# Kernel optimization log

Measured on AMD Instinct MI355X. Metric: run time of the kernel, lower is better.

The kernel has to match this reference:

```python
import jax, jax.numpy as jnp
import numpy as np

EMBED_DIM = 1024
NUM_HEADS = 16
HEAD_DIM = EMBED_DIM // NUM_HEADS
B, T = 4, 1024
NEG = -1.0e9
LN_EPS = 1e-5


def setup_inputs() -> dict:
    key = jax.random.key(0)
    ks = jax.random.split(key, 13)
    s = 1.0 / np.sqrt(EMBED_DIM)
    return {
        "query": jax.random.normal(ks[0], (B, T, EMBED_DIM), jnp.float32),
        "key": jax.random.normal(ks[1], (B, T, EMBED_DIM), jnp.float32),
        "value": jax.random.normal(ks[2], (B, T, EMBED_DIM), jnp.float32),
        "mask": jax.random.randint(ks[3], (B, 1, T, T), 0, 2, jnp.int32),
        "Wq": jax.random.normal(ks[4], (EMBED_DIM, EMBED_DIM), jnp.float32) * s,
        "bq": jnp.zeros((EMBED_DIM,), jnp.float32),
        "Wk": jax.random.normal(ks[5], (EMBED_DIM, EMBED_DIM), jnp.float32) * s,
        "bk": jnp.zeros((EMBED_DIM,), jnp.float32),
        "Wv": jax.random.normal(ks[6], (EMBED_DIM, EMBED_DIM), jnp.float32) * s,
        "bv": jnp.zeros((EMBED_DIM,), jnp.float32),
        "Wo": jax.random.normal(ks[7], (EMBED_DIM, EMBED_DIM), jnp.float32) * s,
        "bo": jnp.zeros((EMBED_DIM,), jnp.float32),
        "gamma": jnp.ones((EMBED_DIM,), jnp.float32),
        "beta": jnp.zeros((EMBED_DIM,), jnp.float32),
    }


def _split_heads(x):
    # (B, T, E) -> (B, H, T, D)
    b, t, _ = x.shape
    return x.reshape(b, t, NUM_HEADS, HEAD_DIM).transpose(0, 2, 1, 3)


def _mha(query, key, value, mask, Wq, bq, Wk, bk, Wv, bv, Wo, bo, gamma, beta,
         temperature=1.0):
    q = _split_heads(query @ Wq.T + bq)
    k = _split_heads(key @ Wk.T + bk)
    v = _split_heads(value @ Wv.T + bv)
    # scores: (B, H, T, T)
    scale = jnp.sqrt(jnp.float32(HEAD_DIM)) * temperature
    scores = jnp.einsum("bhqd,bhkd->bhqk", q, k) / scale
    scores = jnp.where(mask == 0, NEG, scores)
    scores = scores - jnp.max(scores, axis=-1, keepdims=True)
    # temperature >= 0.01 in this config, so the low-temperature hard-cutoff
    # branch is skipped (matches torch's Python-level `if temperature < 0.01`).
    scores = jnp.nan_to_num(scores, nan=0.0, posinf=1.0e9, neginf=-1.0e9)
    attn = jax.nn.softmax(scores, axis=-1)
    # eval mode: dropout is identity (self.training is False)
    out = jnp.einsum("bhqk,bhkd->bhqd", attn, v)  # (B, H, T, D)
    out = out.transpose(0, 2, 1, 3).reshape(query.shape[0], query.shape[1], EMBED_DIM)
    out = out @ Wo.T + bo
    # layer norm over embed_dim
    mu = jnp.mean(out, axis=-1, keepdims=True)
    var = jnp.mean(jnp.square(out - mu), axis=-1, keepdims=True)
    out = (out - mu) * jax.lax.rsqrt(var + LN_EPS) * gamma + beta
    return out


def reference(query, key, value, mask, Wq, bq, Wk, bk, Wv, bv, Wo, bo, gamma, beta):
    return _mha(query, key, value, mask, Wq, bq, Wk, bk, Wv, bv, Wo, bo, gamma, beta)
```

## Files before the change

kernel.cpp:

```cpp
#include <hip/hip_runtime.h>
#include <cmath>

#define T_SEQ 1024
#define EMB   1024
#define NH    16
#define HD    64
#define NB    4
#define BQ    64
#define BK    64

#define QSCALE 0.18033688011112042f
#define BIAS2  -1.44269504e9f

using frag8   = __attribute__((ext_vector_type(8))) short;
using f32x4   = __attribute__((ext_vector_type(4))) float;
using short4v = __attribute__((ext_vector_type(4))) short;
using short8v = __attribute__((ext_vector_type(8))) short;

__device__ inline short f2bf(float f) {
    union { float f; unsigned u; } x; x.f = f;
    unsigned r = (x.u + 0x7FFFu + ((x.u >> 16) & 1u)) >> 16;
    return (short)r;
}
__device__ inline short f2bf_rhu(float f) {
    union { float f; unsigned u; } x; x.f = f;
    return (short)((x.u + 0x8000u) >> 16);
}
__device__ inline float bf2f(unsigned short u) {
    union { unsigned u; float f; } x; x.u = ((unsigned)u) << 16;
    return x.f;
}

__device__ inline void glds16(const short* g, short* l) {
    __builtin_amdgcn_global_load_lds(
        (const __attribute__((address_space(1))) void*)g,
        (__attribute__((address_space(3))) void*)l, 16, 0, 0);
}

struct ConvArgs { const void* src[8]; short* dst[8]; int n8[8]; };

__global__ __launch_bounds__(256) void convert_bf16(ConvArgs a) {
    const int y = blockIdx.y;
    const int t = blockIdx.x * 256 + threadIdx.x;
    if (t >= a.n8[y]) return;
    if (y == 7) {
        const short BB = f2bf(BIAS2);
        const int base = t * 8;
        const int rlo0 = base & 15;
        const int clm  = (base >> 4) & 15;
        const int c16  = (base >> 8) & 63;
        const int rt16 = (base >> 14) & 63;
        const int bb   = base >> 20;
        const int col  = c16 * 16 + clm;
        const int row0 = rt16 * 16 + rlo0;
        const int* mi = (const int*)a.src[7] + ((size_t)bb * T_SEQ + row0) * T_SEQ + col;
        short8v o;
#pragma unroll
        for (int jj = 0; jj < 8; ++jj)
            o[jj] = mi[(size_t)jj * T_SEQ] ? (short)0 : BB;
        *(short8v*)&a.dst[7][base] = o;
        return;
    }
    const float4* s = (const float4*)a.src[y];
    const float4 v0 = s[t * 2], v1 = s[t * 2 + 1];
    short8v o;
    o[0] = f2bf(v0.x); o[1] = f2bf(v0.y); o[2] = f2bf(v0.z); o[3] = f2bf(v0.w);
    o[4] = f2bf(v1.x); o[5] = f2bf(v1.y); o[6] = f2bf(v1.z); o[7] = f2bf(v1.w);
    *(short8v*)&a.dst[y][t * 8] = o;
}

struct GemmB { const short* A; const short* W; const float* bias; short* out; float scale; };
struct QkvArgs { GemmB g[3]; };

template <int MODE>
__device__ inline void gemm_core(const short* __restrict__ A,
                                 const short* __restrict__ W,
                                 const float* __restrict__ bias,
                                 float scale,
                                 short* __restrict__ outS,
                                 float* __restrict__ outF)
{
    __shared__ short As[128 * 32];
    __shared__ short Bs[128 * 32];

    const int tid  = threadIdx.x;
    const int wave = tid >> 6;
    const int lane = tid & 63;
    const int quad = lane >> 4;
    const int lm   = lane & 15;
    const int wr   = wave >> 1;
    const int wc   = wave & 1;

    const int m0 = blockIdx.y * 128;
    const int n0 = blockIdx.x * 128;
    const int K  = EMB;

    const int G0 = wave * 64 + lane, G1 = G0 + 256;
    const short* aSrc0 = A + (size_t)(m0 + (G0 >> 2)) * K + (G0 & 3) * 8;
    const short* aSrc1 = A + (size_t)(m0 + (G1 >> 2)) * K + (G1 & 3) * 8;
    const short* bSrc0 = W + (size_t)(n0 + (G0 >> 2)) * K + (G0 & 3) * 8;
    const short* bSrc1 = W + (size_t)(n0 + (G1 >> 2)) * K + (G1 & 3) * 8;
    short* aDst0 = As + wave * 512;
    short* aDst1 = As + 2048 + wave * 512;
    short* bDst0 = Bs + wave * 512;
    short* bDst1 = Bs + 2048 + wave * 512;

    f32x4 acc[4][4];
#pragma unroll
    for (int i = 0; i < 4; ++i)
#pragma unroll
        for (int j = 0; j < 4; ++j) acc[i][j] = (f32x4){0.f, 0.f, 0.f, 0.f};

    for (int kk = 0; kk < K; kk += 32) {
        __syncthreads();
        glds16(aSrc0 + kk, aDst0);
        glds16(aSrc1 + kk, aDst1);
        glds16(bSrc0 + kk, bDst0);
        glds16(bSrc1 + kk, bDst1);
        __syncthreads();

        frag8 aF[4], bF[4];
#pragma unroll
        for (int i = 0; i < 4; ++i)
            aF[i] = *(const frag8*)&As[(wr * 64 + i * 16 + lm) * 32 + quad * 8];
#pragma unroll
        for (int j = 0; j < 4; ++j)
            bF[j] = *(const frag8*)&Bs[(wc * 64 + j * 16 + lm) * 32 + quad * 8];
#pragma unroll
        for (int i = 0; i < 4; ++i)
#pragma unroll
            for (int j = 0; j < 4; ++j)
                acc[i][j] = __builtin_amdgcn_mfma_f32_16x16x32_bf16(
                    aF[i], bF[j], acc[i][j], 0, 0, 0);
    }

#pragma unroll
    for (int i = 0; i < 4; ++i)
#pragma unroll
        for (int j = 0; j < 4; ++j) {
            const int n = n0 + wc * 64 + j * 16 + lm;
            const float bv = bias[n];
#pragma unroll
            for (int rr = 0; rr < 4; ++rr) {
                const int m = m0 + wr * 64 + i * 16 + quad * 4 + rr;
                const float val = (acc[i][j][rr] + bv) * scale;
                if (MODE == 0) {
                    outF[(size_t)m * EMB + n] = val;
                } else {
                    const int bb = m >> 10, tt = m & 1023;
                    const int h = n >> 6,  d  = n & 63;
                    const size_t bh = (size_t)bb * NH + h;
                    if (MODE == 1) {
                        outS[((bh * 64 + (tt >> 4)) * 8 + (d >> 3)) * 128 +
                             (tt & 15) * 8 + (d & 7)] = f2bf(val);
                    } else {
                        outS[((((bh * 16 + (tt >> 6)) * 2 + ((tt >> 5) & 1)) * 4 +
                              (d >> 4)) * 4 + ((tt >> 3) & 3)) * 128 +
                             (d & 15) * 8 + (tt & 7)] = f2bf(val);
                    }
                }
            }
        }
}

__global__ __launch_bounds__(256) void gemm_qkv(QkvArgs args) {
    const GemmB g = args.g[blockIdx.z];
    if (blockIdx.z < 2) gemm_core<1>(g.A, g.W, g.bias, g.scale, g.out, nullptr);
    else                gemm_core<2>(g.A, g.W, g.bias, g.scale, g.out, nullptr);
}

__global__ __launch_bounds__(256) void gemm_wo(const short* __restrict__ A,
                                               const short* __restrict__ W,
                                               const float* __restrict__ bias,
                                               float* __restrict__ out) {
    gemm_core<0>(A, W, bias, 1.0f, nullptr, out);
}

__global__ __launch_bounds__(256, 4) void flash_attn_mfma(
    const short* __restrict__ qf_, const short* __restrict__ kf_,
    const short* __restrict__ vf_, const short* __restrict__ mf_,
    short* __restrict__ out)
{
    __shared__ short Pl[4][2][16][72];

    const int tid  = threadIdx.x;
    const int wave = tid >> 6;
    const int lane = tid & 63;
    const int quad = lane >> 4;
    const int lm   = lane & 15;

    const int b  = blockIdx.z, h = blockIdx.y;
    const int q0 = blockIdx.x * BQ;
    const size_t bh = (size_t)b * NH + h;

    const short* qb_ = qf_ + (bh * 64 + (q0 >> 4) + wave) * 1024;
    const frag8 qfa = *(const frag8*)&qb_[(quad * 16 + lm) * 8];
    const frag8 qfb = *(const frag8*)&qb_[((quad + 4) * 16 + lm) * 8];

    const short* mrow = mf_ + ((size_t)b * 64 + (q0 >> 4) + wave) * (64 * 256)
                        + lm * 16 + quad * 4;

    f32x4 of[4];
#pragma unroll
    for (int dc = 0; dc < 4; ++dc) of[dc] = (f32x4){0.f, 0.f, 0.f, 0.f};
    float lsum[4] = {0.f, 0.f, 0.f, 0.f};

    for (int kt2 = 0; kt2 < T_SEQ / BK; ++kt2) {
        const int pp = kt2 & 1;

        frag8 vf[2][4];
        const short* vbase = vf_ + (bh * 16 + kt2) * 4096;
#pragma unroll
        for (int kh2 = 0; kh2 < 2; ++kh2)
#pragma unroll
            for (int dc = 0; dc < 4; ++dc)
                vf[kh2][dc] = *(const frag8*)
                    &vbase[((kh2 * 4 + dc) * 4 + quad) * 128 + lm * 8];

        short4v mb[4];
#pragma unroll
        for (int kc = 0; kc < 4; ++kc)
            mb[kc] = *(const short4v*)&mrow[(kt2 * 4 + kc) * 256];

        f32x4 s[4];
#pragma unroll
        for (int kc = 0; kc < 4; ++kc) {
            const short* kbase = kf_ + (bh * 64 + kt2 * 4 + kc) * 1024;
            const frag8 kfa = *(const frag8*)&kbase[(quad * 16 + lm) * 8];
            const frag8 kfb = *(const frag8*)&kbase[((quad + 4) * 16 + lm) * 8];
            f32x4 a = (f32x4){ bf2f((unsigned short)mb[kc][0]),
                               bf2f((unsigned short)mb[kc][1]),
                               bf2f((unsigned short)mb[kc][2]),
                               bf2f((unsigned short)mb[kc][3]) };
            a = __builtin_amdgcn_mfma_f32_16x16x32_bf16(qfa, kfa, a, 0, 0, 0);
            a = __builtin_amdgcn_mfma_f32_16x16x32_bf16(qfb, kfb, a, 0, 0, 0);
            s[kc] = a;
        }

#pragma unroll
        for (int kc = 0; kc < 4; ++kc)
#pragma unroll
            for (int r = 0; r < 4; ++r) {
                const float p = exp2f(s[kc][r]);
                lsum[r] += p;
                Pl[wave][pp][quad * 4 + r][kc * 16 + lm] = f2bf_rhu(p);
            }

        const frag8 pfa = *(const frag8*)&Pl[wave][pp][lm][quad * 8];
        const frag8 pfb = *(const frag8*)&Pl[wave][pp][lm][32 + quad * 8];
#pragma unroll
        for (int dc = 0; dc < 4; ++dc) {
            of[dc] = __builtin_amdgcn_mfma_f32_16x16x32_bf16(pfa, vf[0][dc], of[dc], 0, 0, 0);
            of[dc] = __builtin_amdgcn_mfma_f32_16x16x32_bf16(pfb, vf[1][dc], of[dc], 0, 0, 0);
        }
    }

#pragma unroll
    for (int r = 0; r < 4; ++r) {
        lsum[r] += __shfl_xor(lsum[r], 1);
        lsum[r] += __shfl_xor(lsum[r], 2);
        lsum[r] += __shfl_xor(lsum[r], 4);
        lsum[r] += __shfl_xor(lsum[r], 8);
    }
    float inv[4];
#pragma unroll
    for (int r = 0; r < 4; ++r) inv[r] = 1.0f / lsum[r];

    short* ob = out + ((size_t)b * T_SEQ + q0 + wave * 16) * EMB + h * HD;
#pragma unroll
    for (int dc = 0; dc < 4; ++dc)
#pragma unroll
        for (int r = 0; r < 4; ++r)
            ob[(size_t)(quad * 4 + r) * EMB + dc * 16 + lm] = f2bf(of[dc][r] * inv[r]);
}

__global__ __launch_bounds__(256) void layernorm_k(
    const float* __restrict__ x, const float* __restrict__ gamma,
    const float* __restrict__ beta, float* __restrict__ out)
{
    __shared__ float ws1[4], ws2[4];
    const int tid = threadIdx.x;
    const size_t row = blockIdx.x;

    const float4 v = *(const float4*)&x[row * EMB + tid * 4];
    float s  = v.x + v.y + v.z + v.w;
    float ss = v.x * v.x + v.y * v.y + v.z * v.z + v.w * v.w;
#pragma unroll
    for (int off = 32; off > 0; off >>= 1) {
        s  += __shfl_down(s, off);
        ss += __shfl_down(ss, off);
    }
    if ((tid & 63) == 0) { ws1[tid >> 6] = s; ws2[tid >> 6] = ss; }
    __syncthreads();
    if (tid == 0) {
        const float a = ws1[0] + ws1[1] + ws1[2] + ws1[3];
        const float bsum = ws2[0] + ws2[1] + ws2[2] + ws2[3];
        const float mu = a * (1.0f / EMB);
        const float var = bsum * (1.0f / EMB) - mu * mu;
        ws1[0] = mu;
        ws2[0] = rsqrtf(var + 1e-5f);
    }
    __syncthreads();
    const float mu = ws1[0], rstd = ws2[0];

    const float4 g = *(const float4*)&gamma[tid * 4];
    const float4 bt = *(const float4*)&beta[tid * 4];
    float4 r;
    r.x = (v.x - mu) * rstd * g.x + bt.x;
    r.y = (v.y - mu) * rstd * g.y + bt.y;
    r.z = (v.z - mu) * rstd * g.z + bt.z;
    r.w = (v.w - mu) * rstd * g.w + bt.w;
    *(float4*)&out[row * EMB + tid * 4] = r;
}

extern "C" void kernel_launch(void* const* d_in, const int* in_sizes, int n_in,
                              void* d_out, int out_size, void* d_ws, size_t ws_size,
                              hipStream_t stream) {
    const float* query = (const float*)d_in[0];
    const float* key_i = (const float*)d_in[1];
    const float* value = (const float*)d_in[2];
    const int*   mask  = (const int*)d_in[3];
    const float* Wq = (const float*)d_in[4];
    const float* bq = (const float*)d_in[5];
    const float* Wk = (const float*)d_in[6];
    const float* bk = (const float*)d_in[7];
    const float* Wv = (const float*)d_in[8];
    const float* bv = (const float*)d_in[9];
    const float* Wo = (const float*)d_in[10];
    const float* bo = (const float*)d_in[11];
    const float* gamma = (const float*)d_in[12];
    const float* beta  = (const float*)d_in[13];

    const size_t SZ = (size_t)NB * T_SEQ * EMB;
    const size_t WZ = (size_t)EMB * EMB;
    short* sws = (short*)d_ws;
    short* q_bf  = sws;
    short* k_bf  = sws + SZ;
    short* v_bf  = sws + 2 * SZ;
    short* w_bf  = sws + 3 * SZ;
    short* qh    = sws + 4 * SZ;
    short* kh    = sws + 5 * SZ;
    short* vh    = sws + 6 * SZ;
    short* maskb = sws + 7 * SZ;
    short* attnb = q_bf;
    float* projb = (float*)(sws + SZ);

    ConvArgs ca;
    ca.src[0] = query; ca.dst[0] = q_bf;          ca.n8[0] = (int)(SZ / 8);
    ca.src[1] = key_i; ca.dst[1] = k_bf;          ca.n8[1] = (int)(SZ / 8);
    ca.src[2] = value; ca.dst[2] = v_bf;          ca.n8[2] = (int)(SZ / 8);
    ca.src[3] = Wq;    ca.dst[3] = w_bf;          ca.n8[3] = (int)(WZ / 8);
    ca.src[4] = Wk;    ca.dst[4] = w_bf + WZ;     ca.n8[4] = (int)(WZ / 8);
    ca.src[5] = Wv;    ca.dst[5] = w_bf + 2 * WZ; ca.n8[5] = (int)(WZ / 8);
    ca.src[6] = Wo;    ca.dst[6] = w_bf + 3 * WZ; ca.n8[6] = (int)(WZ / 8);
    ca.src[7] = mask;  ca.dst[7] = maskb;         ca.n8[7] = (int)(SZ / 8);
    convert_bf16<<<dim3((SZ / 8 + 255) / 256, 8), 256, 0, stream>>>(ca);

    QkvArgs qa;
    qa.g[0] = { q_bf, w_bf,          bq, qh, QSCALE };
    qa.g[1] = { k_bf, w_bf + WZ,     bk, kh, 1.0f };
    qa.g[2] = { v_bf, w_bf + 2 * WZ, bv, vh, 1.0f };
    gemm_qkv<<<dim3(EMB / 128, NB * T_SEQ / 128, 3), 256, 0, stream>>>(qa);

    flash_attn_mfma<<<dim3(T_SEQ / BQ, NH, NB), 256, 0, stream>>>(qh, kh, vh, maskb, attnb);

    gemm_wo<<<dim3(EMB / 128, NB * T_SEQ / 128), 256, 0, stream>>>(
        attnb, w_bf + 3 * WZ, bo, projb);

    layernorm_k<<<dim3(NB * T_SEQ), 256, 0, stream>>>(projb, gamma, beta, (float*)d_out);
}
```

Before: 268.5 us.

## Coalesce mask conversion, remap GEMM block order, and tile-layout GEMM outputs

Moves mask conversion into its own kernel that reads int4 rows coalesced and scatters into the 16x16 tile layout, in place of strided per-column reads. The QKV and Wo GEMMs now permute block IDs to group tiles for better L2 reuse across CUs/XCDs. The GEMM epilogues write in an MFMA-fragment-friendly layout: Q/K so attention loads fragments with a new offset, Wo output in 16x16 tiles that layernorm reads back. Output stores become more contiguous per lane, at the cost of scattered 2-byte mask stores and a more complex addressing scheme.

```diff
diff --git a/kernel.cpp b/kernel.cpp
--- a/kernel.cpp
+++ b/kernel.cpp
@@ -37,30 +37,12 @@
         (__attribute__((address_space(3))) void*)l, 16, 0, 0);
 }
 
-struct ConvArgs { const void* src[8]; short* dst[8]; int n8[8]; };
+struct ConvArgs { const float* src[7]; short* dst[7]; int n8[7]; };
 
 __global__ __launch_bounds__(256) void convert_bf16(ConvArgs a) {
     const int y = blockIdx.y;
     const int t = blockIdx.x * 256 + threadIdx.x;
     if (t >= a.n8[y]) return;
-    if (y == 7) {
-        const short BB = f2bf(BIAS2);
-        const int base = t * 8;
-        const int rlo0 = base & 15;
-        const int clm  = (base >> 4) & 15;
-        const int c16  = (base >> 8) & 63;
-        const int rt16 = (base >> 14) & 63;
-        const int bb   = base >> 20;
-        const int col  = c16 * 16 + clm;
-        const int row0 = rt16 * 16 + rlo0;
-        const int* mi = (const int*)a.src[7] + ((size_t)bb * T_SEQ + row0) * T_SEQ + col;
-        short8v o;
-#pragma unroll
-        for (int jj = 0; jj < 8; ++jj)
-            o[jj] = mi[(size_t)jj * T_SEQ] ? (short)0 : BB;
-        *(short8v*)&a.dst[7][base] = o;
-        return;
-    }
     const float4* s = (const float4*)a.src[y];
     const float4 v0 = s[t * 2], v1 = s[t * 2 + 1];
     short8v o;
@@ -69,6 +51,26 @@
     *(short8v*)&a.dst[y][t * 8] = o;
 }
 
+__global__ __launch_bounds__(256) void convert_mask(
+    const int* __restrict__ mask, short* __restrict__ dst)
+{
+    const int wave = threadIdx.x >> 6, lane = threadIdx.x & 63;
+    const int tile = blockIdx.x * 4 + wave;
+    const int bb   = tile >> 12;
+    const int rt16 = (tile >> 6) & 63;
+    const int c16  = tile & 63;
+    const int row_in = lane >> 2;
+    const int col4   = (lane & 3) * 4;
+    const int4 mv = *(const int4*)&mask[((size_t)bb * T_SEQ + rt16 * 16 + row_in) * T_SEQ
+                                        + c16 * 16 + col4];
+    const short BB = f2bf(BIAS2);
+    short* o = dst + (size_t)tile * 256 + row_in;
+    o[(col4 + 0) * 16] = mv.x ? (short)0 : BB;
+    o[(col4 + 1) * 16] = mv.y ? (short)0 : BB;
+    o[(col4 + 2) * 16] = mv.z ? (short)0 : BB;
+    o[(col4 + 3) * 16] = mv.w ? (short)0 : BB;
+}
+
 struct GemmB { const short* A; const short* W; const float* bias; short* out; float scale; };
 struct QkvArgs { GemmB g[3]; };
 
@@ -78,7 +80,8 @@
                                  const float* __restrict__ bias,
                                  float scale,
                                  short* __restrict__ outS,
-                                 float* __restrict__ outF)
+                                 float* __restrict__ outF,
+                                 int m0, int n0)
 {
     __shared__ short As[128 * 32];
     __shared__ short Bs[128 * 32];
@@ -90,10 +93,7 @@
     const int lm   = lane & 15;
     const int wr   = wave >> 1;
     const int wc   = wave & 1;
-
-    const int m0 = blockIdx.y * 128;
-    const int n0 = blockIdx.x * 128;
-    const int K  = EMB;
+    const int K    = EMB;
 
     const int G0 = wave * 64 + lane, G1 = G0 + 256;
     const short* aSrc0 = A + (size_t)(m0 + (G0 >> 2)) * K + (G0 & 3) * 8;
@@ -145,14 +145,15 @@
                 const int m = m0 + wr * 64 + i * 16 + quad * 4 + rr;
                 const float val = (acc[i][j][rr] + bv) * scale;
                 if (MODE == 0) {
-                    outF[(size_t)m * EMB + n] = val;
+                    outF[((size_t)(m >> 4) * 64 + (n >> 4)) * 256 +
+                         rr * 64 + quad * 16 + lm] = val;
                 } else {
                     const int bb = m >> 10, tt = m & 1023;
                     const int h = n >> 6,  d  = n & 63;
                     const size_t bh = (size_t)bb * NH + h;
                     if (MODE == 1) {
-                        outS[((bh * 64 + (tt >> 4)) * 8 + (d >> 3)) * 128 +
-                             (tt & 15) * 8 + (d & 7)] = f2bf(val);
+                        outS[((bh * 64 + (tt >> 4)) * 4 + (d >> 4)) * 256 +
+                             rr * 64 + quad * 16 + lm] = f2bf(val);
                     } else {
                         outS[((((bh * 16 + (tt >> 6)) * 2 + ((tt >> 5) & 1)) * 4 +
                               (d >> 4)) * 4 + ((tt >> 3) & 3)) * 128 +
@@ -164,16 +165,30 @@
 }
 
 __global__ __launch_bounds__(256) void gemm_qkv(QkvArgs args) {
-    const GemmB g = args.g[blockIdx.z];
-    if (blockIdx.z < 2) gemm_core<1>(g.A, g.W, g.bias, g.scale, g.out, nullptr);
-    else                gemm_core<2>(g.A, g.W, g.bias, g.scale, g.out, nullptr);
+    const int id = blockIdx.x + 8 * blockIdx.y + 256 * blockIdx.z;
+    const int a  = id & 7;
+    const int k2 = id >> 3;
+    const int nb = k2 & 7;
+    const int c  = k2 >> 3;
+    const int pair = a * 12 + c;
+    const int mb = pair & 31;
+    const int zb = pair >> 5;
+    const GemmB g = args.g[zb];
+    if (zb < 2) gemm_core<1>(g.A, g.W, g.bias, g.scale, g.out, nullptr, mb * 128, nb * 128);
+    else        gemm_core<2>(g.A, g.W, g.bias, g.scale, g.out, nullptr, mb * 128, nb * 128);
 }
 
 __global__ __launch_bounds__(256) void gemm_wo(const short* __restrict__ A,
                                                const short* __restrict__ W,
                                                const float* __restrict__ bias,
                                                float* __restrict__ out) {
-    gemm_core<0>(A, W, bias, 1.0f, nullptr, out);
+    const int id = blockIdx.x + 8 * blockIdx.y;
+    const int a  = id & 7;
+    const int k2 = id >> 3;
+    const int nb = k2 & 7;
+    const int c  = k2 >> 3;
+    const int mb = a * 4 + c;
+    gemm_core<0>(A, W, bias, 1.0f, nullptr, out, mb * 128, nb * 128);
 }
 
 __global__ __launch_bounds__(256, 4) void flash_attn_mfma(
@@ -193,9 +208,11 @@
     const int q0 = blockIdx.x * BQ;
     const size_t bh = (size_t)b * NH + h;
 
+    const int foff = (quad >> 1) * 256 + (lm & 3) * 64 + (lm >> 2) * 16 + (quad & 1) * 8;
+
     const short* qb_ = qf_ + (bh * 64 + (q0 >> 4) + wave) * 1024;
-    const frag8 qfa = *(const frag8*)&qb_[(quad * 16 + lm) * 8];
-    const frag8 qfb = *(const frag8*)&qb_[((quad + 4) * 16 + lm) * 8];
+    const frag8 qfa = *(const frag8*)&qb_[foff];
+    const frag8 qfb = *(const frag8*)&qb_[foff + 512];
 
     const short* mrow = mf_ + ((size_t)b * 64 + (q0 >> 4) + wave) * (64 * 256)
                         + lm * 16 + quad * 4;
@@ -226,8 +243,8 @@
 #pragma unroll
         for (int kc = 0; kc < 4; ++kc) {
             const short* kbase = kf_ + (bh * 64 + kt2 * 4 + kc) * 1024;
-            const frag8 kfa = *(const frag8*)&kbase[(quad * 16 + lm) * 8];
-            const frag8 kfb = *(const frag8*)&kbase[((quad + 4) * 16 + lm) * 8];
+            const frag8 kfa = *(const frag8*)&kbase[foff];
+            const frag8 kfb = *(const frag8*)&kbase[foff + 512];
             f32x4 a = (f32x4){ bf2f((unsigned short)mb[kc][0]),
                                bf2f((unsigned short)mb[kc][1]),
                                bf2f((unsigned short)mb[kc][2]),
@@ -280,9 +297,11 @@
 {
     __shared__ float ws1[4], ws2[4];
     const int tid = threadIdx.x;
-    const size_t row = blockIdx.x;
-
-    const float4 v = *(const float4*)&x[row * EMB + tid * 4];
+    const int row = blockIdx.x;
+    const int m16 = row >> 4, rr = row & 3, qd = (row >> 2) & 3;
+
+    const float4 v = *(const float4*)&x[((size_t)m16 * 64 + (tid >> 2)) * 256 +
+                                        rr * 64 + qd * 16 + (tid & 3) * 4];
     float s  = v.x + v.y + v.z + v.w;
     float ss = v.x * v.x + v.y * v.y + v.z * v.z + v.w * v.w;
 #pragma unroll
@@ -310,7 +329,7 @@
     r.y = (v.y - mu) * rstd * g.y + bt.y;
     r.z = (v.z - mu) * rstd * g.z + bt.z;
     r.w = (v.w - mu) * rstd * g.w + bt.w;
-    *(float4*)&out[row * EMB + tid * 4] = r;
+    *(float4*)&out[(size_t)row * EMB + tid * 4] = r;
 }
 
 extern "C" void kernel_launch(void* const* d_in, const int* in_sizes, int n_in,
@@ -353,8 +372,9 @@
     ca.src[4] = Wk;    ca.dst[4] = w_bf + WZ;     ca.n8[4] = (int)(WZ / 8);
     ca.src[5] = Wv;    ca.dst[5] = w_bf + 2 * WZ; ca.n8[5] = (int)(WZ / 8);
     ca.src[6] = Wo;    ca.dst[6] = w_bf + 3 * WZ; ca.n8[6] = (int)(WZ / 8);
-    ca.src[7] = mask;  ca.dst[7] = maskb;         ca.n8[7] = (int)(SZ / 8);
-    convert_bf16<<<dim3((SZ / 8 + 255) / 256, 8), 256, 0, stream>>>(ca);
+    convert_bf16<<<dim3((SZ / 8 + 255) / 256, 7), 256, 0, stream>>>(ca);
+
+    convert_mask<<<dim3(NB * 64 * 64 / 4), 256, 0, stream>>>(mask, maskb);
 
     QkvArgs qa;
     qa.g[0] = { q_bf, w_bf,          bq, qh, QSCALE };
```

Result: slower. 303.5 us (+13.0%).
